# Kernel tuning notes

Hardware: AMD Instinct MI355X
Metric: run time of the kernel (lower is better)

The kernel has to match this reference:

```python
import jax, jax.numpy as jnp
import numpy as np

B, T, C = 2, 2048, 1024
N_HEAD, D_HEAD = 16, 64


def setup_inputs() -> dict:
    key = jax.random.key(0)
    k1, k2, k3 = jax.random.split(key, 3)
    scale_in = 1.0 / np.sqrt(C)
    return {
        "x": jax.random.normal(k1, (B, T, C), dtype=jnp.float32),
        "W_attn": jax.random.normal(k2, (C, 3 * C), dtype=jnp.float32) * scale_in,
        "b_attn": jnp.zeros((3 * C,), dtype=jnp.float32),
        "W_proj": jax.random.normal(k3, (C, C), dtype=jnp.float32) * scale_in,
        "b_proj": jnp.zeros((C,), dtype=jnp.float32),
    }


def reference(x, W_attn, b_attn, W_proj, b_proj):
    Bx, Tx, Cx = x.shape
    qkv = x @ W_attn + b_attn                       # [B,T,3C]
    q, k, v = jnp.split(qkv, 3, axis=-1)
    # [B,T,C] -> [B,H,T,Dh]
    q = q.reshape(Bx, Tx, N_HEAD, D_HEAD).transpose(0, 2, 1, 3)
    k = k.reshape(Bx, Tx, N_HEAD, D_HEAD).transpose(0, 2, 1, 3)
    v = v.reshape(Bx, Tx, N_HEAD, D_HEAD).transpose(0, 2, 1, 3)
    att = jnp.einsum("bhqd,bhkd->bhqk", q, k) * (1.0 / jnp.sqrt(D_HEAD))
    causal_mask = jnp.tril(jnp.ones((Tx, Tx), dtype=jnp.bool_))[None, None]
    att = jnp.where(causal_mask, att, -jnp.inf)
    att = jax.nn.softmax(att, axis=-1)
    y = jnp.einsum("bhqk,bhkd->bhqd", att, v)        # [B,H,T,Dh]
    y = y.transpose(0, 2, 1, 3).reshape(Bx, Tx, Cx)  # [B,T,C]
    return y @ W_proj + b_proj
```

## Files before the change

### kernel.cpp

```cpp
#include <hip/hip_runtime.h>

#define BB 2
#define TT 2048
#define CC 1024
#define NHEAD 16
#define DHEAD 64

typedef __attribute__((ext_vector_type(8))) short short8;
typedef __attribute__((ext_vector_type(8))) unsigned short ushort8;
typedef __attribute__((ext_vector_type(4))) float floatx4;
typedef __attribute__((ext_vector_type(2))) unsigned int uintx2;

__device__ inline unsigned short f32_to_bf16_rne(float f) {
  unsigned u = __builtin_bit_cast(unsigned, f);
  unsigned r = (u + 0x7FFFu + ((u >> 16) & 1u)) >> 16;
  return (unsigned short)r;
}
__device__ inline unsigned cvt_pk_bf16(float lo, float hi) {
  unsigned r;
  asm("v_cvt_pk_bf16_f32 %0, %1, %2" : "=v"(r) : "v"(lo), "v"(hi));
  return r;
}
__device__ inline void gload_lds16(const void* g, void* l) {
  __builtin_amdgcn_global_load_lds(
      (const __attribute__((address_space(1))) void*)g,
      (__attribute__((address_space(3))) void*)l, 16, 0, 0);
}

__device__ inline void transpose_tile(const float* __restrict__ W,
                                      unsigned short* __restrict__ Wt,
                                      int K, int N, int scale_cut, float scl,
                                      int bx, int by, float (*T)[33]) {
  const int tx = threadIdx.x & 31;
  const int ty = threadIdx.x >> 5;
  const int r0 = by * 32, c0 = bx * 32;
#pragma unroll
  for (int i = 0; i < 4; ++i)
    T[ty + i * 8][tx] = W[(size_t)(r0 + ty + i * 8) * N + c0 + tx];
  __syncthreads();
#pragma unroll
  for (int i = 0; i < 4; ++i) {
    const int nrow = c0 + ty + i * 8;
    const float s = (nrow < scale_cut) ? scl : 1.0f;
    Wt[(size_t)nrow * K + r0 + tx] = f32_to_bf16_rne(T[tx][ty + i * 8] * s);
  }
}

__global__ __launch_bounds__(256) void prep_kernel(
    const float* __restrict__ x, const float* __restrict__ W_attn,
    const float* __restrict__ b_attn, const float* __restrict__ W_proj,
    unsigned short* __restrict__ xb, unsigned short* __restrict__ Wat,
    unsigned short* __restrict__ Wpt, float* __restrict__ bscl, float scl) {
  __shared__ float T[32][33];
  const int id = blockIdx.x;
  if (id < 4096) {
    const int i = (id * 256 + threadIdx.x) * 4;
    float4 v = *(const float4*)(x + i);
    ushort4 o;
    o.x = f32_to_bf16_rne(v.x);
    o.y = f32_to_bf16_rne(v.y);
    o.z = f32_to_bf16_rne(v.z);
    o.w = f32_to_bf16_rne(v.w);
    *(ushort4*)(xb + i) = o;
  } else if (id < 4096 + 3072) {
    const int t = id - 4096;
    transpose_tile(W_attn, Wat, CC, 3 * CC, CC, scl, t % 96, t / 96, T);
  } else if (id < 4096 + 3072 + 1024) {
    const int t = id - (4096 + 3072);
    transpose_tile(W_proj, Wpt, CC, CC, 0, 1.0f, t % 32, t / 32, T);
  } else {
    const int i = (id - 8192) * 256 + threadIdx.x;
    if (i < 3 * CC) bscl[i] = b_attn[i] * (i < CC ? scl : 1.0f);
  }
}

__global__ __launch_bounds__(256) void transpose_v_kernel(
    const unsigned short* __restrict__ qkv, unsigned short* __restrict__ vT) {
  __shared__ unsigned short Ts[64][72];
  const int tt0 = blockIdx.x * 64;
  const int bh = blockIdx.y;
  const int h = bh & (NHEAD - 1);
  const int b = bh >> 4;
  const int tid = threadIdx.x;
  const unsigned short* src = qkv + (size_t)(b * TT) * (3 * CC) + 2 * CC + h * DHEAD;
#pragma unroll
  for (int it = 0; it < 2; ++it) {
    const int t = it * 32 + (tid >> 3);
    const int d8 = (tid & 7) * 8;
    ushort8 v = *(const ushort8*)(src + (size_t)(tt0 + t) * (3 * CC) + d8);
#pragma unroll
    for (int j = 0; j < 8; ++j) Ts[t][d8 + j] = v[j];
  }
  __syncthreads();
  unsigned short* dst = vT + ((size_t)((b * NHEAD + h) * DHEAD)) * TT;
#pragma unroll
  for (int it = 0; it < 2; ++it) {
    const int d = it * 32 + (tid >> 3);
    const int t8 = (tid & 7) * 8;
    ushort8 o;
#pragma unroll
    for (int j = 0; j < 8; ++j) o[j] = Ts[t8 + j][d];
    *(ushort8*)(dst + (size_t)d * TT + tt0 + t8) = o;
  }
}

template <bool BF16_OUT, int BN>
__global__ __launch_bounds__(256) void gemm_mfma_kernel(
    const unsigned short* __restrict__ A, const unsigned short* __restrict__ Bt,
    const float* __restrict__ bias, void* __restrict__ Cout,
    int M, int N, int K) {
  constexpr int NR = BN / 32;
  __shared__ unsigned short As[128 * 32];
  __shared__ unsigned short Bs[BN * 32];

  const int tid = threadIdx.x;
  const int wave = tid >> 6;
  const int lane = tid & 63;
  const int row0 = blockIdx.y * 128;
  const int col0 = blockIdx.x * BN;
  const int wr = (wave >> 1) * 64;
  const int wc = (wave & 1) * (BN / 2);

  floatx4 acc[4][NR];
#pragma unroll
  for (int m = 0; m < 4; ++m)
#pragma unroll
    for (int n = 0; n < NR; ++n) acc[m][n] = (floatx4){0.f, 0.f, 0.f, 0.f};

  const int sRow = lane >> 2;
  const int sK = (lane & 3) * 8;

  for (int k0 = 0; k0 < K; k0 += 32) {
#pragma unroll
    for (int c = 0; c < 2; ++c) {
      const int g = c * 4 + wave;
      gload_lds16(A + (size_t)(row0 + g * 16 + sRow) * K + k0 + sK,
                  (char*)As + g * 1024);
    }
    if constexpr (BN == 128) {
#pragma unroll
      for (int c = 0; c < 2; ++c) {
        const int g = c * 4 + wave;
        gload_lds16(Bt + (size_t)(col0 + g * 16 + sRow) * K + k0 + sK,
                    (char*)Bs + g * 1024);
      }
    } else {
      gload_lds16(Bt + (size_t)(col0 + wave * 16 + sRow) * K + k0 + sK,
                  (char*)Bs + wave * 1024);
    }
    __syncthreads();

    short8 af[4], bf[NR];
#pragma unroll
    for (int m = 0; m < 4; ++m)
      af[m] = *(const short8*)(As + (wr + m * 16 + (lane & 15)) * 32 + (lane >> 4) * 8);
#pragma unroll
    for (int n = 0; n < NR; ++n)
      bf[n] = *(const short8*)(Bs + (wc + n * 16 + (lane & 15)) * 32 + (lane >> 4) * 8);
#pragma unroll
    for (int m = 0; m < 4; ++m)
#pragma unroll
      for (int n = 0; n < NR; ++n)
        acc[m][n] = __builtin_amdgcn_mfma_f32_16x16x32_bf16(af[m], bf[n], acc[m][n], 0, 0, 0);
    __syncthreads();
  }

  const int cl = lane & 15;
  const int rg = (lane >> 4) * 4;
#pragma unroll
  for (int m = 0; m < 4; ++m) {
#pragma unroll
    for (int n = 0; n < NR; ++n) {
      const int col = col0 + wc + n * 16 + cl;
      const float bv = bias[col];
#pragma unroll
      for (int r = 0; r < 4; ++r) {
        const int row = row0 + wr + m * 16 + rg + r;
        const float v = acc[m][n][r] + bv;
        if (BF16_OUT)
          ((unsigned short*)Cout)[(size_t)row * N + col] = f32_to_bf16_rne(v);
        else
          ((float*)Cout)[(size_t)row * N + col] = v;
      }
    }
  }
}

__global__ __launch_bounds__(256) void flash_mfma_kernel(
    const unsigned short* __restrict__ qkv,
    const unsigned short* __restrict__ vT,
    unsigned short* __restrict__ y) {
  __shared__ unsigned short Ks[2][64 * 64];
  __shared__ unsigned short Vs[2][64 * 64];
  __shared__ unsigned short Ps[4][16 * 64];

  const int id = blockIdx.x;
  const int xcd = id & 7;
  const int grp = (id >> 3) & 3;
  const int p = id >> 5;
  const int bh = xcd * 4 + grp;
  const int qtA = 31 - p, qtB = p;
  const int ntA = qtA + 1, ntB = qtB + 1;

  const int h = bh & (NHEAD - 1);
  const int b = bh >> 4;
  const int tid = threadIdx.x;
  const int wq = tid >> 6;
  const int lane = tid & 63;
  const int l15 = lane & 15;
  const int l4 = lane >> 4;
  const int srow = lane >> 3;
  const int schunk = lane & 7;

  const size_t baseQ = (size_t)(b * TT) * (3 * CC) + h * DHEAD;
  const size_t baseK = baseQ + CC;
  const size_t vbase = (size_t)((b * NHEAD + h) * DHEAD) * TT;

  short8 aqA[2], aqB[2];
  {
    const unsigned short* qp =
        qkv + baseQ + (size_t)(qtA * 64 + wq * 16 + l15) * (3 * CC) + l4 * 8;
    aqA[0] = *(const short8*)(qp);
    aqA[1] = *(const short8*)(qp + 32);
    const unsigned short* qp2 =
        qkv + baseQ + (size_t)(qtB * 64 + wq * 16 + l15) * (3 * CC) + l4 * 8;
    aqB[0] = *(const short8*)(qp2);
    aqB[1] = *(const short8*)(qp2 + 32);
  }

  floatx4 accT[4];
  float m_i = -1e30f, l_i = 0.f;
#pragma unroll
  for (int n = 0; n < 4; ++n) accT[n] = (floatx4){0.f, 0.f, 0.f, 0.f};

  auto stage = [&](int KT, int BUF) {
#pragma unroll
    for (int it = 0; it < 2; ++it) {
      const int blk = it * 4 + wq;
      const int grow = blk * 8 + srow;
      gload_lds16(qkv + baseK + (size_t)(KT * 64 + grow) * (3 * CC) +
                      (schunk ^ srow) * 8,
                  (char*)Ks[BUF] + blk * 1024);
      gload_lds16(vT + vbase + (size_t)grow * TT + KT * 64 + (schunk ^ srow) * 8,
                  (char*)Vs[BUF] + blk * 1024);
    }
  };

  auto epilogue = [&](int qt) {
    char* Pw = (char*)Ps[wq];
    const float inv = 1.0f / l_i;
#pragma unroll
    for (int nd = 0; nd < 4; ++nd) {
      uintx2 dw;
      dw[0] = cvt_pk_bf16(accT[nd][0] * inv, accT[nd][1] * inv);
      dw[1] = cvt_pk_bf16(accT[nd][2] * inv, accT[nd][3] * inv);
      const int c = nd * 2 + (l4 >> 1);
      *(uintx2*)(Pw + l15 * 128 + ((c ^ (l15 & 7)) * 16) + (l4 & 1) * 8) = dw;
    }
    asm volatile("s_waitcnt lgkmcnt(0)" ::: "memory");
#pragma unroll
    for (int ch = 0; ch < 2; ++ch) {
      const int q16 = lane >> 2;
      const int c = ch * 4 + (lane & 3);
      ushort8 o = *(const ushort8*)(Pw + q16 * 128 + ((c ^ (q16 & 7)) * 16));
      const int qg = qt * 64 + wq * 16 + q16;
      *(ushort8*)(y + (size_t)(b * TT + qg) * CC + h * DHEAD + c * 8) = o;
    }
  };

  const int nt_total = ntA + ntB;

  stage(0, 0);
  asm volatile("s_waitcnt vmcnt(0)" ::: "memory");
  __builtin_amdgcn_s_barrier();

  for (int t = 0; t < nt_total; ++t) {
    const bool phB = (t >= ntA);
    const int kt = phB ? t - ntA : t;
    const int qminw = (phB ? qtB : qtA) * 64 + wq * 16;
    const int cur = t & 1;
    if (t + 1 < nt_total)
      stage((t + 1 >= ntA) ? t + 1 - ntA : t + 1, cur ^ 1);

    floatx4 sa[4];
#pragma unroll
    for (int f = 0; f < 4; ++f) sa[f] = (floatx4){0.f, 0.f, 0.f, 0.f};

    __builtin_amdgcn_s_setprio(1);
#pragma unroll
    for (int kc = 0; kc < 2; ++kc) {
      const short8 aq = phB ? aqB[kc] : aqA[kc];
#pragma unroll
      for (int f = 0; f < 4; ++f) {
        const int row = 16 * f + l15;
        short8 bk = *(const short8*)(Ks[cur] + row * 64 +
                                     ((kc * 4 + l4) ^ (row & 7)) * 8);
        sa[f] = __builtin_amdgcn_mfma_f32_16x16x32_bf16(bk, aq, sa[f], 0, 0, 0);
      }
    }
    __builtin_amdgcn_s_setprio(0);

    const int qg = qminw + l15;
    if (kt * 64 + 63 > qminw) {
#pragma unroll
      for (int f = 0; f < 4; ++f)
#pragma unroll
        for (int r = 0; r < 4; ++r) {
          const int kg = kt * 64 + f * 16 + l4 * 4 + r;
          if (kg > qg) sa[f][r] = -1e30f;
        }
    }
    float rm = -1e30f;
#pragma unroll
    for (int f = 0; f < 4; ++f)
      rm = fmaxf(rm, fmaxf(fmaxf(sa[f][0], sa[f][1]), fmaxf(sa[f][2], sa[f][3])));
    rm = fmaxf(rm, __shfl_xor(rm, 16, 64));
    rm = fmaxf(rm, __shfl_xor(rm, 32, 64));

    float rs = 0.f;
    if (__all(rm <= m_i + 8.0f)) {
#pragma unroll
      for (int f = 0; f < 4; ++f)
#pragma unroll
        for (int r = 0; r < 4; ++r) {
          const float pv = __builtin_amdgcn_exp2f(sa[f][r] - m_i);
          sa[f][r] = pv;
          rs += pv;
        }
      rs += __shfl_xor(rs, 16, 64);
      rs += __shfl_xor(rs, 32, 64);
      l_i += rs;
    } else {
      const float mn = fmaxf(m_i, rm);
      const float scale = __builtin_amdgcn_exp2f(m_i - mn);
#pragma unroll
      for (int f = 0; f < 4; ++f)
#pragma unroll
        for (int r = 0; r < 4; ++r) {
          const float pv = __builtin_amdgcn_exp2f(sa[f][r] - mn);
          sa[f][r] = pv;
          rs += pv;
        }
      rs += __shfl_xor(rs, 16, 64);
      rs += __shfl_xor(rs, 32, 64);
      l_i = l_i * scale + rs;
      m_i = mn;
#pragma unroll
      for (int nd = 0; nd < 4; ++nd) accT[nd] *= scale;
    }

    char* Pg = (char*)Ps[wq];
#pragma unroll
    for (int f = 0; f < 4; ++f) {
      uintx2 dw;
      dw[0] = cvt_pk_bf16(sa[f][0], sa[f][1]);
      dw[1] = cvt_pk_bf16(sa[f][2], sa[f][3]);
      const int c = f * 2 + (l4 >> 1);
      *(uintx2*)(Pg + l15 * 128 + ((c ^ (l15 & 7)) * 16) + (l4 & 1) * 8) = dw;
    }
    asm volatile("s_waitcnt lgkmcnt(0)" ::: "memory");

    short8 pb[2];
#pragma unroll
    for (int kc = 0; kc < 2; ++kc) {
      const int c = kc * 4 + l4;
      pb[kc] = *(const short8*)(Pg + l15 * 128 + ((c ^ (l15 & 7)) * 16));
    }

    __builtin_amdgcn_s_setprio(1);
#pragma unroll
    for (int kc = 0; kc < 2; ++kc) {
#pragma unroll
      for (int nd = 0; nd < 4; ++nd) {
        const int row = 16 * nd + l15;
        short8 vb = *(const short8*)(Vs[cur] + row * 64 +
                                     ((kc * 4 + l4) ^ (row & 7)) * 8);
        accT[nd] = __builtin_amdgcn_mfma_f32_16x16x32_bf16(vb, pb[kc], accT[nd], 0, 0, 0);
      }
    }
    __builtin_amdgcn_s_setprio(0);

    asm volatile("s_waitcnt vmcnt(0)" ::: "memory");
    __builtin_amdgcn_s_barrier();

    if (t == ntA - 1) {
      epilogue(qtA);
      m_i = -1e30f;
      l_i = 0.f;
#pragma unroll
      for (int n = 0; n < 4; ++n) accT[n] = (floatx4){0.f, 0.f, 0.f, 0.f};
    }
  }

  epilogue(qtB);
}

extern "C" void kernel_launch(void* const* d_in, const int* in_sizes, int n_in,
                              void* d_out, int out_size, void* d_ws, size_t ws_size,
                              hipStream_t stream) {
  const float* x      = (const float*)d_in[0];
  const float* W_attn = (const float*)d_in[1];
  const float* b_attn = (const float*)d_in[2];
  const float* W_proj = (const float*)d_in[3];
  const float* b_proj = (const float*)d_in[4];
  float* out = (float*)d_out;

  const int M = BB * TT;
  const float SCL = 0.125f * 1.44269504089f;

  unsigned short* qkvb = (unsigned short*)d_ws;
  unsigned short* xb   = qkvb + (size_t)M * 3 * CC;
  unsigned short* Wat  = xb + (size_t)M * CC;
  unsigned short* Wpt  = Wat + (size_t)3 * CC * CC;
  unsigned short* yb   = Wpt + (size_t)CC * CC;
  unsigned short* vTb  = yb + (size_t)M * CC;
  float* bscl = (float*)(vTb + (size_t)BB * NHEAD * DHEAD * TT);

  prep_kernel<<<8204, 256, 0, stream>>>(x, W_attn, b_attn, W_proj,
                                        xb, Wat, Wpt, bscl, SCL);

  {
    dim3 grid((3 * CC) / 128, M / 128);
    gemm_mfma_kernel<true, 128><<<grid, 256, 0, stream>>>(xb, Wat, bscl, qkvb, M, 3 * CC, CC);
  }

  {
    dim3 grid(TT / 64, BB * NHEAD);
    transpose_v_kernel<<<grid, 256, 0, stream>>>(qkvb, vTb);
  }

  flash_mfma_kernel<<<512, 256, 0, stream>>>(qkvb, vTb, yb);

  {
    dim3 grid(CC / 64, M / 128);
    gemm_mfma_kernel<false, 64><<<grid, 256, 0, stream>>>(yb, Wpt, b_proj, out, M, CC, CC);
  }
}
```

Before: 123.4 us.

## Fold V transpose into QKV GEMM epilogue and deepen K step to 64

Removes the separate transpose_v kernel. For column tiles that hold V, the QKV GEMM epilogue now stages the tile transposed in swizzled LDS and writes it directly to the vT layout. This saves a launch and a read and write of V. The GEMM main loop also loads two 32-wide K chunks per barrier pair, which halves the number of syncs at the cost of more LDS per block. V tiles skip writing V into qkv, which is fine only if the flash kernel reads V from vT alone.

```diff
diff --git a/kernel.cpp b/kernel.cpp
--- a/kernel.cpp
+++ b/kernel.cpp
@@ -74,44 +74,15 @@
   }
 }
 
-__global__ __launch_bounds__(256) void transpose_v_kernel(
-    const unsigned short* __restrict__ qkv, unsigned short* __restrict__ vT) {
-  __shared__ unsigned short Ts[64][72];
-  const int tt0 = blockIdx.x * 64;
-  const int bh = blockIdx.y;
-  const int h = bh & (NHEAD - 1);
-  const int b = bh >> 4;
-  const int tid = threadIdx.x;
-  const unsigned short* src = qkv + (size_t)(b * TT) * (3 * CC) + 2 * CC + h * DHEAD;
-#pragma unroll
-  for (int it = 0; it < 2; ++it) {
-    const int t = it * 32 + (tid >> 3);
-    const int d8 = (tid & 7) * 8;
-    ushort8 v = *(const ushort8*)(src + (size_t)(tt0 + t) * (3 * CC) + d8);
-#pragma unroll
-    for (int j = 0; j < 8; ++j) Ts[t][d8 + j] = v[j];
-  }
-  __syncthreads();
-  unsigned short* dst = vT + ((size_t)((b * NHEAD + h) * DHEAD)) * TT;
-#pragma unroll
-  for (int it = 0; it < 2; ++it) {
-    const int d = it * 32 + (tid >> 3);
-    const int t8 = (tid & 7) * 8;
-    ushort8 o;
-#pragma unroll
-    for (int j = 0; j < 8; ++j) o[j] = Ts[t8 + j][d];
-    *(ushort8*)(dst + (size_t)d * TT + tt0 + t8) = o;
-  }
-}
-
-template <bool BF16_OUT, int BN>
+template <bool BF16_OUT, int BN, bool VFOLD>
 __global__ __launch_bounds__(256) void gemm_mfma_kernel(
     const unsigned short* __restrict__ A, const unsigned short* __restrict__ Bt,
     const float* __restrict__ bias, void* __restrict__ Cout,
-    int M, int N, int K) {
+    unsigned short* __restrict__ vTp, int M, int N, int K) {
   constexpr int NR = BN / 32;
-  __shared__ unsigned short As[128 * 32];
-  __shared__ unsigned short Bs[BN * 32];
+  __shared__ unsigned short SM[128 * 64 + BN * 64];
+  unsigned short* As = SM;
+  unsigned short* Bs = SM + 128 * 64;
 
   const int tid = threadIdx.x;
   const int wave = tid >> 6;
@@ -130,57 +101,98 @@
   const int sRow = lane >> 2;
   const int sK = (lane & 3) * 8;
 
-  for (int k0 = 0; k0 < K; k0 += 32) {
-#pragma unroll
-    for (int c = 0; c < 2; ++c) {
-      const int g = c * 4 + wave;
-      gload_lds16(A + (size_t)(row0 + g * 16 + sRow) * K + k0 + sK,
-                  (char*)As + g * 1024);
-    }
-    if constexpr (BN == 128) {
+  for (int k0 = 0; k0 < K; k0 += 64) {
+#pragma unroll
+    for (int kc = 0; kc < 2; ++kc) {
 #pragma unroll
       for (int c = 0; c < 2; ++c) {
         const int g = c * 4 + wave;
-        gload_lds16(Bt + (size_t)(col0 + g * 16 + sRow) * K + k0 + sK,
-                    (char*)Bs + g * 1024);
-      }
-    } else {
-      gload_lds16(Bt + (size_t)(col0 + wave * 16 + sRow) * K + k0 + sK,
-                  (char*)Bs + wave * 1024);
+        gload_lds16(A + (size_t)(row0 + g * 16 + sRow) * K + k0 + kc * 32 + sK,
+                    (char*)As + kc * 8192 + g * 1024);
+      }
+      if constexpr (BN == 128) {
+#pragma unroll
+        for (int c = 0; c < 2; ++c) {
+          const int g = c * 4 + wave;
+          gload_lds16(Bt + (size_t)(col0 + g * 16 + sRow) * K + k0 + kc * 32 + sK,
+                      (char*)Bs + kc * 8192 + g * 1024);
+        }
+      } else {
+        gload_lds16(Bt + (size_t)(col0 + wave * 16 + sRow) * K + k0 + kc * 32 + sK,
+                    (char*)Bs + kc * 4096 + wave * 1024);
+      }
     }
     __syncthreads();
 
-    short8 af[4], bf[NR];
-#pragma unroll
-    for (int m = 0; m < 4; ++m)
-      af[m] = *(const short8*)(As + (wr + m * 16 + (lane & 15)) * 32 + (lane >> 4) * 8);
-#pragma unroll
-    for (int n = 0; n < NR; ++n)
-      bf[n] = *(const short8*)(Bs + (wc + n * 16 + (lane & 15)) * 32 + (lane >> 4) * 8);
-#pragma unroll
-    for (int m = 0; m < 4; ++m)
+#pragma unroll
+    for (int kc = 0; kc < 2; ++kc) {
+      short8 af[4], bf[NR];
+#pragma unroll
+      for (int m = 0; m < 4; ++m)
+        af[m] = *(const short8*)(As + kc * 4096 +
+                                 (wr + m * 16 + (lane & 15)) * 32 + (lane >> 4) * 8);
 #pragma unroll
       for (int n = 0; n < NR; ++n)
-        acc[m][n] = __builtin_amdgcn_mfma_f32_16x16x32_bf16(af[m], bf[n], acc[m][n], 0, 0, 0);
+        bf[n] = *(const short8*)(Bs + kc * (BN * 32) +
+                                 (wc + n * 16 + (lane & 15)) * 32 + (lane >> 4) * 8);
+#pragma unroll
+      for (int m = 0; m < 4; ++m)
+#pragma unroll
+        for (int n = 0; n < NR; ++n)
+          acc[m][n] = __builtin_amdgcn_mfma_f32_16x16x32_bf16(af[m], bf[n], acc[m][n], 0, 0, 0);
+    }
     __syncthreads();
   }
 
   const int cl = lane & 15;
   const int rg = (lane >> 4) * 4;
-#pragma unroll
-  for (int m = 0; m < 4; ++m) {
-#pragma unroll
-    for (int n = 0; n < NR; ++n) {
-      const int col = col0 + wc + n * 16 + cl;
-      const float bv = bias[col];
-#pragma unroll
-      for (int r = 0; r < 4; ++r) {
-        const int row = row0 + wr + m * 16 + rg + r;
-        const float v = acc[m][n][r] + bv;
-        if (BF16_OUT)
-          ((unsigned short*)Cout)[(size_t)row * N + col] = f32_to_bf16_rne(v);
-        else
-          ((float*)Cout)[(size_t)row * N + col] = v;
+
+  if (VFOLD && col0 >= 2 * CC) {
+    unsigned short* T = SM;
+#pragma unroll
+    for (int m = 0; m < 4; ++m) {
+#pragma unroll
+      for (int n = 0; n < 4; ++n) {
+        const int c = wc + n * 16 + cl;
+        const float bsv = bias[col0 + c];
+        const int tok0 = wr + m * 16 + rg;
+        const int swz = (cl) << 3;
+        const unsigned w0 = cvt_pk_bf16(acc[m][n][0] + bsv, acc[m][n][1] + bsv);
+        const unsigned w1 = cvt_pk_bf16(acc[m][n][2] + bsv, acc[m][n][3] + bsv);
+        *(unsigned*)(T + c * 128 + (((tok0 & 0x78) ^ swz) | (tok0 & 7))) = w0;
+        *(unsigned*)(T + c * 128 + ((((tok0 + 2) & 0x78) ^ swz) | ((tok0 + 2) & 7))) = w1;
+      }
+    }
+    __syncthreads();
+    const int bb = row0 >> 11;
+    const int rloc = row0 & (TT - 1);
+#pragma unroll
+    for (int i = 0; i < 8; ++i) {
+      const int idx = i * 256 + tid;
+      const int c = idx >> 4;
+      const int g = idx & 15;
+      const int gcol = col0 + c;
+      const int hh = (gcol >> 6) & (NHEAD - 1);
+      const int dd = gcol & (DHEAD - 1);
+      ushort8 o = *(const ushort8*)(T + c * 128 + ((g ^ (c & 15)) << 3));
+      *(ushort8*)(vTp + ((size_t)((bb * NHEAD + hh) * DHEAD + dd)) * TT + rloc + g * 8) = o;
+    }
+  } else {
+#pragma unroll
+    for (int m = 0; m < 4; ++m) {
+#pragma unroll
+      for (int n = 0; n < NR; ++n) {
+        const int col = col0 + wc + n * 16 + cl;
+        const float bv = bias[col];
+#pragma unroll
+        for (int r = 0; r < 4; ++r) {
+          const int row = row0 + wr + m * 16 + rg + r;
+          const float v = acc[m][n][r] + bv;
+          if (BF16_OUT)
+            ((unsigned short*)Cout)[(size_t)row * N + col] = f32_to_bf16_rne(v);
+          else
+            ((float*)Cout)[(size_t)row * N + col] = v;
+        }
       }
     }
   }
@@ -421,18 +433,15 @@
 
   {
     dim3 grid((3 * CC) / 128, M / 128);
-    gemm_mfma_kernel<true, 128><<<grid, 256, 0, stream>>>(xb, Wat, bscl, qkvb, M, 3 * CC, CC);
-  }
-
-  {
-    dim3 grid(TT / 64, BB * NHEAD);
-    transpose_v_kernel<<<grid, 256, 0, stream>>>(qkvb, vTb);
+    gemm_mfma_kernel<true, 128, true><<<grid, 256, 0, stream>>>(
+        xb, Wat, bscl, qkvb, vTb, M, 3 * CC, CC);
   }
 
   flash_mfma_kernel<<<512, 256, 0, stream>>>(qkvb, vTb, yb);
 
   {
     dim3 grid(CC / 64, M / 128);
-    gemm_mfma_kernel<false, 64><<<grid, 256, 0, stream>>>(yb, Wpt, b_proj, out, M, CC, CC);
-  }
-}
+    gemm_mfma_kernel<false, 64, false><<<grid, 256, 0, stream>>>(
+        yb, Wpt, b_proj, out, nullptr, M, CC, CC);
+  }
+}
```

After: 121.6 us. Within noise of the previous version (-1.4%).

## Add 256x256 triple-buffered swizzled GEMM for QKV projection, widen K step in proj GEMM

Applied to the files above, without the earlier changes.

Replaces the 128x128 QKV GEMM with a new 512-thread kernel using 256x256 tiles, triple-buffered LDS staging via global_load_lds, an XOR swizzle against bank conflicts, split A/B prefetch interleaved with MFMA phases, setprio, and an XCD-aware block-to-tile mapping. The output-projection GEMM now stages 64 K per sync instead of 32, halving barrier count. The aim is better data reuse and overlap of loads with MFMA work. The trade-off is fewer blocks (192) and a large LDS footprint per block, which limits occupancy and load balance.

```diff
diff --git a/kernel.cpp b/kernel.cpp
--- a/kernel.cpp
+++ b/kernel.cpp
@@ -104,14 +104,139 @@
   }
 }
 
+__global__ __launch_bounds__(512, 2) void gemm256_kernel(
+    const unsigned short* __restrict__ A,
+    const unsigned short* __restrict__ Bt,
+    const float* __restrict__ bias,
+    unsigned short* __restrict__ C,
+    int M, int N, int K) {
+  __shared__ unsigned short SA[3][256 * 32];
+  __shared__ unsigned short SB[3][256 * 32];
+
+  const int id = blockIdx.x;
+  const int xcd = id & 7;
+  const int j = id >> 3;
+  const int row0 = (xcd * 2 + (j >= 12 ? 1 : 0)) * 256;
+  const int col0 = (j % 12) * 256;
+
+  const int tid = threadIdx.x;
+  const int w = tid >> 6;
+  const int lane = tid & 63;
+  const int l15 = lane & 15;
+  const int l4 = lane >> 4;
+  const int wr = (w >> 2) * 128;
+  const int wc = (w & 3) * 64;
+  const int sr = lane >> 2;
+  const int sc = lane & 3;
+
+  floatx4 acc[8][4];
+#pragma unroll
+  for (int m = 0; m < 8; ++m)
+#pragma unroll
+    for (int n = 0; n < 4; ++n) acc[m][n] = (floatx4){0.f, 0.f, 0.f, 0.f};
+
+  auto stageA = [&](int t) {
+    const int buf = t % 3;
+    const int k0 = t * 32;
+#pragma unroll
+    for (int l = 0; l < 2; ++l) {
+      const int r = w * 16 + sr + l * 128;
+      gload_lds16(A + (size_t)(row0 + r) * K + k0 + ((sc ^ ((r >> 1) & 3)) * 8),
+                  (char*)SA[buf] + (w * 16 + l * 128) * 64);
+    }
+  };
+  auto stageB = [&](int t) {
+    const int buf = t % 3;
+    const int k0 = t * 32;
+#pragma unroll
+    for (int l = 0; l < 2; ++l) {
+      const int r = w * 16 + sr + l * 128;
+      gload_lds16(Bt + (size_t)(col0 + r) * K + k0 + ((sc ^ ((r >> 1) & 3)) * 8),
+                  (char*)SB[buf] + (w * 16 + l * 128) * 64);
+    }
+  };
+
+  stageA(0); stageB(0);
+  stageA(1); stageB(1);
+  asm volatile("s_waitcnt vmcnt(4)" ::: "memory");
+  __builtin_amdgcn_s_barrier();
+
+  const int NT = K / 32;
+  for (int t = 0; t < NT; ++t) {
+    const unsigned short* sa = SA[t % 3];
+    const unsigned short* sb = SB[t % 3];
+
+    short8 af[4], bf[4];
+#pragma unroll
+    for (int n = 0; n < 4; ++n) {
+      const int rb = wc + n * 16 + l15;
+      bf[n] = *(const short8*)(sb + rb * 32 + ((l4 ^ ((rb >> 1) & 3)) * 8));
+    }
+#pragma unroll
+    for (int m = 0; m < 4; ++m) {
+      const int ra = wr + m * 16 + l15;
+      af[m] = *(const short8*)(sa + ra * 32 + ((l4 ^ ((ra >> 1) & 3)) * 8));
+    }
+    if (t + 2 < NT) stageA(t + 2);
+    __builtin_amdgcn_s_barrier();
+    __builtin_amdgcn_s_setprio(1);
+#pragma unroll
+    for (int m = 0; m < 4; ++m)
+#pragma unroll
+      for (int n = 0; n < 4; ++n)
+        acc[m][n] = __builtin_amdgcn_mfma_f32_16x16x32_bf16(af[m], bf[n], acc[m][n], 0, 0, 0);
+    __builtin_amdgcn_s_setprio(0);
+    __builtin_amdgcn_s_barrier();
+
+#pragma unroll
+    for (int m = 0; m < 4; ++m) {
+      const int ra = wr + 64 + m * 16 + l15;
+      af[m] = *(const short8*)(sa + ra * 32 + ((l4 ^ ((ra >> 1) & 3)) * 8));
+    }
+    if (t + 2 < NT) stageB(t + 2);
+    __builtin_amdgcn_s_barrier();
+    __builtin_amdgcn_s_setprio(1);
+#pragma unroll
+    for (int m = 0; m < 4; ++m)
+#pragma unroll
+      for (int n = 0; n < 4; ++n)
+        acc[4 + m][n] = __builtin_amdgcn_mfma_f32_16x16x32_bf16(af[m], bf[n], acc[4 + m][n], 0, 0, 0);
+    __builtin_amdgcn_s_setprio(0);
+    __builtin_amdgcn_s_barrier();
+
+    if (t + 1 < NT) {
+      if (t + 2 < NT)
+        asm volatile("s_waitcnt vmcnt(4)" ::: "memory");
+      else
+        asm volatile("s_waitcnt vmcnt(0)" ::: "memory");
+      __builtin_amdgcn_s_barrier();
+    }
+  }
+
+  const int rg = l4 * 4;
+#pragma unroll
+  for (int m = 0; m < 8; ++m) {
+#pragma unroll
+    for (int n = 0; n < 4; ++n) {
+      const int col = col0 + wc + n * 16 + l15;
+      const float bv = bias[col];
+#pragma unroll
+      for (int r = 0; r < 4; ++r) {
+        const int row = row0 + wr + m * 16 + rg + r;
+        C[(size_t)row * N + col] = f32_to_bf16_rne(acc[m][n][r] + bv);
+      }
+    }
+  }
+}
+
 template <bool BF16_OUT, int BN>
 __global__ __launch_bounds__(256) void gemm_mfma_kernel(
     const unsigned short* __restrict__ A, const unsigned short* __restrict__ Bt,
     const float* __restrict__ bias, void* __restrict__ Cout,
     int M, int N, int K) {
   constexpr int NR = BN / 32;
-  __shared__ unsigned short As[128 * 32];
-  __shared__ unsigned short Bs[BN * 32];
+  __shared__ unsigned short As[128 * 64];
+  __shared__ unsigned short Bs[BN * 64];
 
   const int tid = threadIdx.x;
   const int wave = tid >> 6;
@@ -130,38 +255,46 @@
   const int sRow = lane >> 2;
   const int sK = (lane & 3) * 8;
 
-  for (int k0 = 0; k0 < K; k0 += 32) {
-#pragma unroll
-    for (int c = 0; c < 2; ++c) {
-      const int g = c * 4 + wave;
-      gload_lds16(A + (size_t)(row0 + g * 16 + sRow) * K + k0 + sK,
-                  (char*)As + g * 1024);
-    }
-    if constexpr (BN == 128) {
+  for (int k0 = 0; k0 < K; k0 += 64) {
+#pragma unroll
+    for (int kc = 0; kc < 2; ++kc) {
 #pragma unroll
       for (int c = 0; c < 2; ++c) {
         const int g = c * 4 + wave;
-        gload_lds16(Bt + (size_t)(col0 + g * 16 + sRow) * K + k0 + sK,
-                    (char*)Bs + g * 1024);
+        gload_lds16(A + (size_t)(row0 + g * 16 + sRow) * K + k0 + kc * 32 + sK,
+                    (char*)As + kc * 8192 + g * 1024);
       }
-    } else {
-      gload_lds16(Bt + (size_t)(col0 + wave * 16 + sRow) * K + k0 + sK,
-                  (char*)Bs + wave * 1024);
+      if constexpr (BN == 128) {
+#pragma unroll
+        for (int c = 0; c < 2; ++c) {
+          const int g = c * 4 + wave;
+          gload_lds16(Bt + (size_t)(col0 + g * 16 + sRow) * K + k0 + kc * 32 + sK,
+                      (char*)Bs + kc * 8192 + g * 1024);
+        }
+      } else {
+        gload_lds16(Bt + (size_t)(col0 + wave * 16 + sRow) * K + k0 + kc * 32 + sK,
+                    (char*)Bs + kc * 4096 + wave * 1024);
+      }
     }
     __syncthreads();
 
-    short8 af[4], bf[NR];
-#pragma unroll
-    for (int m = 0; m < 4; ++m)
-      af[m] = *(const short8*)(As + (wr + m * 16 + (lane & 15)) * 32 + (lane >> 4) * 8);
-#pragma unroll
-    for (int n = 0; n < NR; ++n)
-      bf[n] = *(const short8*)(Bs + (wc + n * 16 + (lane & 15)) * 32 + (lane >> 4) * 8);
-#pragma unroll
-    for (int m = 0; m < 4; ++m)
+#pragma unroll
+    for (int kc = 0; kc < 2; ++kc) {
+      short8 af[4], bf[NR];
+#pragma unroll
+      for (int m = 0; m < 4; ++m)
+        af[m] = *(const short8*)(As + kc * 4096 +
+                                 (wr + m * 16 + (lane & 15)) * 32 + (lane >> 4) * 8);
 #pragma unroll
       for (int n = 0; n < NR; ++n)
-        acc[m][n] = __builtin_amdgcn_mfma_f32_16x16x32_bf16(af[m], bf[n], acc[m][n], 0, 0, 0);
+        bf[n] = *(const short8*)(Bs + kc * (BN * 32) +
+                                 (wc + n * 16 + (lane & 15)) * 32 + (lane >> 4) * 8);
+#pragma unroll
+      for (int m = 0; m < 4; ++m)
+#pragma unroll
+        for (int n = 0; n < NR; ++n)
+          acc[m][n] = __builtin_amdgcn_mfma_f32_16x16x32_bf16(af[m], bf[n], acc[m][n], 0, 0, 0);
+    }
     __syncthreads();
   }
 
@@ -419,10 +552,7 @@
   prep_kernel<<<8204, 256, 0, stream>>>(x, W_attn, b_attn, W_proj,
                                         xb, Wat, Wpt, bscl, SCL);
 
-  {
-    dim3 grid((3 * CC) / 128, M / 128);
-    gemm_mfma_kernel<true, 128><<<grid, 256, 0, stream>>>(xb, Wat, bscl, qkvb, M, 3 * CC, CC);
-  }
+  gemm256_kernel<<<192, 512, 0, stream>>>(xb, Wat, bscl, qkvb, M, 3 * CC, CC);
 
   {
     dim3 grid(TT / 64, BB * NHEAD);
@@ -433,6 +563,7 @@
 
   {
     dim3 grid(CC / 64, M / 128);
-    gemm_mfma_kernel<false, 64><<<grid, 256, 0, stream>>>(yb, Wpt, b_proj, out, M, CC, CC);
-  }
-}
+    gemm_mfma_kernel<false, 64><<<grid, 256, 0, stream>>>(
+        yb, Wpt, b_proj, out, M, CC, CC);
+  }
+}
```

Result: faster. 120.4 us (-2.4%).
